# Optimization experiments

Measured on AMD Instinct MI355X. Metric: run time of the kernel, lower is better.

Reference implementation:

```python
import jax, jax.numpy as jnp
import numpy as np

EMBED = 1024
HEADS = 16
HEAD_DIM = EMBED // HEADS


def setup_inputs() -> dict:
    key = jax.random.key(0)
    ks = jax.random.split(key, 8)
    N, S = 4, 2048
    inp = {
        "values": jax.random.normal(ks[0], (N, S, EMBED), dtype=jnp.float32),
        "keys": jax.random.normal(ks[1], (N, S, EMBED), dtype=jnp.float32),
        "queries": jax.random.normal(ks[2], (N, S, EMBED), dtype=jnp.float32),
        # Linear weights stored as [in, out] (torch Linear applies x @ W.T; here W already transposed)
        "W_v": jax.random.normal(ks[3], (EMBED, EMBED), dtype=jnp.float32) / np.sqrt(EMBED),
        "W_k": jax.random.normal(ks[4], (EMBED, EMBED), dtype=jnp.float32) / np.sqrt(EMBED),
        "W_q": jax.random.normal(ks[5], (EMBED, EMBED), dtype=jnp.float32) / np.sqrt(EMBED),
        "W_o": jax.random.normal(ks[6], (EMBED, EMBED), dtype=jnp.float32) / np.sqrt(EMBED),
        "b_o": jax.random.normal(ks[7], (EMBED,), dtype=jnp.float32) * 0.01,
    }
    return inp


def reference(values, keys, queries, W_v, W_k, W_q, W_o, b_o):
    N, q_len, _ = queries.shape
    v = (values @ W_v).reshape(N, -1, HEADS, HEAD_DIM)   # [n, v_len, h, d]
    k = (keys @ W_k).reshape(N, -1, HEADS, HEAD_DIM)     # [n, k_len, h, d]
    q = (queries @ W_q).reshape(N, -1, HEADS, HEAD_DIM)  # [n, q_len, h, d]
    # NOTE: original scales by sqrt(embed_size), not sqrt(head_dim)
    energy = jnp.einsum('nqhd,nkhd->nhqk', q, k) / jnp.sqrt(jnp.float32(EMBED))
    attn = jax.nn.softmax(energy, axis=-1)
    out = jnp.einsum('nhqk,nkhd->nqhd', attn, v).reshape(N, q_len, EMBED)
    return out @ W_o + b_o
```

## Files before the change

kernel.cpp:

```cpp
#include <hip/hip_runtime.h>
#include <hip/hip_bf16.h>
#include <stdint.h>

typedef __attribute__((ext_vector_type(8))) short short8;
typedef __attribute__((ext_vector_type(4))) float f32x4;
typedef unsigned short u16;

#define EMBED 1024
#define SEQ 2048
#define NBATCH 4
#define MROWS (NBATCH * SEQ)

__device__ __forceinline__ u16 f2bf(float f) {
  union { float f; uint32_t u; } v; v.f = f;
  uint32_t r = v.u + 0x7fffu + ((v.u >> 16) & 1u);
  return (u16)(r >> 16);
}

__device__ __forceinline__ uint32_t cvtpk(float lo, float hi) {
  uint32_t r;
  asm("v_cvt_pk_bf16_f32 %0, %1, %2" : "=v"(r) : "v"(lo), "v"(hi));
  return r;
}

__device__ __forceinline__ float vexp2(float x) {
  float r;
  asm("v_exp_f32 %0, %1" : "=v"(r) : "v"(x));
  return r;
}

__device__ __forceinline__ void gld16(const void* g, void* l) {
  __builtin_amdgcn_global_load_lds((const __attribute__((address_space(1))) void*)g,
                                   (__attribute__((address_space(3))) void*)l, 16, 0, 0);
}

__global__ __launch_bounds__(256) void wtrans_kernel(const float* __restrict__ W0,
                                                     const float* __restrict__ W1,
                                                     const float* __restrict__ W2,
                                                     const float* __restrict__ W3,
                                                     u16* __restrict__ T0,
                                                     u16* __restrict__ T1,
                                                     u16* __restrict__ T2,
                                                     u16* __restrict__ T3) {
  int z = blockIdx.z;
  const float* W = z == 0 ? W0 : (z == 1 ? W1 : (z == 2 ? W2 : W3));
  u16* Wt = z == 0 ? T0 : (z == 1 ? T1 : (z == 2 ? T2 : T3));
  __shared__ float tile[32][33];
  int bx = blockIdx.x * 32, by = blockIdx.y * 32;
  int tx = threadIdx.x & 31, ty = threadIdx.x >> 5;
#pragma unroll
  for (int i = 0; i < 32; i += 8)
    tile[ty + i][tx] = W[(size_t)(by + ty + i) * EMBED + bx + tx];
  __syncthreads();
#pragma unroll
  for (int i = 0; i < 32; i += 8)
    Wt[(size_t)(bx + ty + i) * EMBED + by + tx] = f2bf(tile[tx][ty + i]);
}

template <int EPI, bool AF32>
__global__ __launch_bounds__(256) void gemm_bt(const void* __restrict__ Av,
                                               const u16* __restrict__ Bt,
                                               void* __restrict__ outp,
                                               const float* __restrict__ bias,
                                               float oscale) {
  constexpr int K = 1024;
  __shared__ u16 lsA[128 * 64];
  __shared__ u16 lsB[128 * 64];
  const int t = threadIdx.x, l = t & 63, w = t >> 6;
  const int g = l >> 4, r15 = l & 15;
  const int m0 = blockIdx.y * 128, n0 = blockIdx.x * 128;
  const int wm = (w >> 1) * 64, wn = (w & 1) * 64;
  f32x4 acc[4][4] = {};
  const int srow = t >> 3;
  const int sc16 = (t & 7) * 16;

  const u16* Bp[4];
#pragma unroll
  for (int j = 0; j < 4; ++j) {
    int row = srow + j * 32;
    int colswz = (sc16 ^ ((row & 7) << 4)) >> 1;
    Bp[j] = Bt + (size_t)(n0 + row) * K + colswz;
  }

  const u16* Ap[4];
  const float* pA[4];
  float4 ar[4][2];
#pragma unroll
  for (int j = 0; j < 4; ++j) {
    int row = srow + j * 32;
    if (AF32) {
      pA[j] = (const float*)Av + (size_t)(m0 + row) * K + (t & 7) * 8;
    } else {
      int colswz = (sc16 ^ ((row & 7) << 4)) >> 1;
      Ap[j] = (const u16*)Av + (size_t)(m0 + row) * K + colswz;
    }
  }

  auto ALOAD = [&](int k0) {
#pragma unroll
    for (int j = 0; j < 4; ++j) {
      ar[j][0] = *(const float4*)(pA[j] + k0);
      ar[j][1] = *(const float4*)(pA[j] + k0 + 4);
    }
  };
  auto AWRITE = [&]() {
#pragma unroll
    for (int j = 0; j < 4; ++j) {
      int row = srow + j * 32;
      uint4 wv = { cvtpk(ar[j][0].x, ar[j][0].y), cvtpk(ar[j][0].z, ar[j][0].w),
                   cvtpk(ar[j][1].x, ar[j][1].y), cvtpk(ar[j][1].z, ar[j][1].w) };
      *(uint4*)((char*)lsA + row * 128 + (sc16 ^ ((row & 7) << 4))) = wv;
    }
  };

  if (AF32) ALOAD(0);

  for (int k0 = 0; k0 < K; k0 += 64) {
#pragma unroll
    for (int j = 0; j < 4; ++j)
      gld16(Bp[j] + k0, lsB + j * 2048 + w * 512);
    if (AF32) {
      AWRITE();
    } else {
#pragma unroll
      for (int j = 0; j < 4; ++j)
        gld16(Ap[j] + k0, lsA + j * 2048 + w * 512);
    }
    __syncthreads();
    short8 af[2][4], bfv[2][4];
#pragma unroll
    for (int kk = 0; kk < 2; ++kk) {
#pragma unroll
      for (int mi = 0; mi < 4; ++mi) {
        int row = wm + mi * 16 + r15;
        af[kk][mi] = *(const short8*)((const char*)lsA + row * 128 + ((kk * 64 + g * 16) ^ ((row & 7) << 4)));
      }
#pragma unroll
      for (int ni = 0; ni < 4; ++ni) {
        int row = wn + ni * 16 + r15;
        bfv[kk][ni] = *(const short8*)((const char*)lsB + row * 128 + ((kk * 64 + g * 16) ^ ((row & 7) << 4)));
      }
    }
    if (AF32 && k0 + 64 < K) ALOAD(k0 + 64);
#pragma unroll
    for (int kk = 0; kk < 2; ++kk)
#pragma unroll
      for (int mi = 0; mi < 4; ++mi)
#pragma unroll
        for (int ni = 0; ni < 4; ++ni)
          acc[mi][ni] = __builtin_amdgcn_mfma_f32_16x16x32_bf16(af[kk][mi], bfv[kk][ni], acc[mi][ni], 0, 0, 0);
    __syncthreads();
  }

#pragma unroll
  for (int mi = 0; mi < 4; ++mi)
#pragma unroll
    for (int ni = 0; ni < 4; ++ni)
#pragma unroll
      for (int r = 0; r < 4; ++r) {
        int row = m0 + wm + mi * 16 + g * 4 + r;
        int col = n0 + wn + ni * 16 + r15;
        float v = acc[mi][ni][r];
        if (EPI == 0) {
          ((u16*)outp)[(((size_t)(row >> 11) * 16 + (col >> 6)) * SEQ + (row & 2047)) * 64 + (col & 63)] = f2bf(v * oscale);
        } else if (EPI == 1) {
          ((u16*)outp)[(((size_t)(row >> 11) * 16 + (col >> 6)) * 64 + (col & 63)) * SEQ + (row & 2047)] = f2bf(v);
        } else {
          ((float*)outp)[(size_t)row * EMBED + col] = v + bias[col];
        }
      }
}

__global__ __launch_bounds__(256) void attn_kernel(const u16* __restrict__ Q,
                                                   const u16* __restrict__ Kb,
                                                   const u16* __restrict__ Vt,
                                                   u16* __restrict__ AO) {
  __shared__ u16 lsK[2][64 * 64];
  __shared__ u16 lsV[2][64 * 64];
  const int t = threadIdx.x, l = t & 63, w = t >> 6;
  const int g = l >> 4, r15 = l & 15;

  const int flat = blockIdx.x;
  const int work = (flat & 7) * 128 + (flat >> 3);
  const int bh = work >> 4;
  const int q0 = (work & 15) * 128;

  const u16* Qh = Q + (size_t)bh * SEQ * 64;
  const u16* Kh = Kb + (size_t)bh * SEQ * 64;
  const u16* Vh = Vt + (size_t)bh * 64 * SEQ;

  short8 qf[2][2];
#pragma unroll
  for (int qi = 0; qi < 2; ++qi)
#pragma unroll
    for (int dh = 0; dh < 2; ++dh)
      qf[qi][dh] = *(const short8*)&Qh[(size_t)(q0 + w * 32 + qi * 16 + r15) * 64 + dh * 32 + g * 8];

  const short8 kones = { 0x3F80, 0x3F80, 0x3F80, 0x3F80, 0x3F80, 0x3F80, 0x3F80, 0x3F80 };
  f32x4 ssum[2] = {};
  f32x4 oacc[4][2] = {};

  const int srow = t >> 3;
  const int scolb = (t & 7) * 16;

  uint4 vreg[2];

  auto STAGE_K = [&](int buf, int kv0) {
#pragma unroll
    for (int j = 0; j < 2; ++j) {
      int row = j * 32 + srow;
      int colswz = (scolb ^ ((row & 7) << 4)) >> 1;
      gld16(Kh + (size_t)(kv0 + row) * 64 + colswz, &lsK[buf][j * 2048 + w * 512]);
    }
  };
  auto VLOAD = [&](int kv0) {
#pragma unroll
    for (int j = 0; j < 2; ++j) {
      int row = j * 32 + srow;
      vreg[j] = *(const uint4*)(Vh + (size_t)row * SEQ + kv0 + (scolb >> 1));
    }
  };
  auto VSTORE = [&](int buf) {
#pragma unroll
    for (int j = 0; j < 2; ++j) {
      int row = j * 32 + srow;
      int c4 = (row & 7) << 4, c3 = ((row >> 3) & 1) << 3;
      char* base = (char*)&lsV[buf][0] + row * 128 + (scolb ^ c4);
      *(uint2*)(base + c3)       = make_uint2(vreg[j].x, vreg[j].y);
      *(uint2*)(base + (8 ^ c3)) = make_uint2(vreg[j].z, vreg[j].w);
    }
  };

  auto STEP = [&](int buf, bool pre, int a) {
    if (pre) {
      VLOAD((a + 1) * 64);
      STAGE_K(buf ^ 1, (a + 1) * 64);
    }
    const u16* Kc = lsK[buf];
    const u16* Vc = lsV[buf];

    f32x4 sacc[2][4] = {};
    __builtin_amdgcn_s_setprio(1);
#pragma unroll
    for (int c = 0; c < 4; ++c) {
      int krow = c * 16 + r15;
      int sz = (krow & 7) << 4;
#pragma unroll
      for (int dh = 0; dh < 2; ++dh) {
        short8 kf = *(const short8*)((const char*)Kc + krow * 128 + ((dh * 64 + g * 16) ^ sz));
#pragma unroll
        for (int qi = 0; qi < 2; ++qi)
          sacc[qi][c] = __builtin_amdgcn_mfma_f32_16x16x32_bf16(kf, qf[qi][dh], sacc[qi][c], 0, 0, 0);
      }
    }
    __builtin_amdgcn_s_setprio(0);

    short8 pb[2][2];
#pragma unroll
    for (int qi = 0; qi < 2; ++qi) {
#pragma unroll
      for (int c = 0; c < 4; ++c)
#pragma unroll
        for (int r = 0; r < 4; ++r)
          sacc[qi][c][r] = vexp2(sacc[qi][c][r]);
#pragma unroll
      for (int kh = 0; kh < 2; ++kh) {
        union { uint32_t u[4]; short8 s; } pu;
        pu.u[0] = cvtpk(sacc[qi][2 * kh][0],     sacc[qi][2 * kh][1]);
        pu.u[1] = cvtpk(sacc[qi][2 * kh][2],     sacc[qi][2 * kh][3]);
        pu.u[2] = cvtpk(sacc[qi][2 * kh + 1][0], sacc[qi][2 * kh + 1][1]);
        pu.u[3] = cvtpk(sacc[qi][2 * kh + 1][2], sacc[qi][2 * kh + 1][3]);
        pb[qi][kh] = pu.s;
      }
    }

#pragma unroll
    for (int qi = 0; qi < 2; ++qi)
#pragma unroll
      for (int kh = 0; kh < 2; ++kh)
        ssum[qi] = __builtin_amdgcn_mfma_f32_16x16x32_bf16(kones, pb[qi][kh], ssum[qi], 0, 0, 0);

    __builtin_amdgcn_s_setprio(1);
#pragma unroll
    for (int dc = 0; dc < 4; ++dc) {
      int vrow = dc * 16 + r15;
      int sz = ((vrow & 7) << 4) | (((vrow >> 3) & 1) << 3);
      const char* vb = (const char*)Vc + vrow * 128;
#pragma unroll
      for (int kh = 0; kh < 2; ++kh) {
        union { uint2 v[2]; short8 s; } va;
        va.v[0] = *(const uint2*)(vb + ((kh * 64 + 8 * g) ^ sz));
        va.v[1] = *(const uint2*)(vb + ((kh * 64 + 32 + 8 * g) ^ sz));
#pragma unroll
        for (int qi = 0; qi < 2; ++qi)
          oacc[dc][qi] = __builtin_amdgcn_mfma_f32_16x16x32_bf16(va.s, pb[qi][kh], oacc[dc][qi], 0, 0, 0);
      }
    }
    __builtin_amdgcn_s_setprio(0);

    if (pre) VSTORE(buf ^ 1);
    __syncthreads();
  };

  VLOAD(0);
  STAGE_K(0, 0);
  VSTORE(0);
  __syncthreads();

#pragma unroll 1
  for (int pair = 0; pair < 16; ++pair) {
    STEP(0, true, 2 * pair);
    STEP(1, pair != 15, 2 * pair + 1);
  }

  const int nb = bh >> 4, h = bh & 15;
  float inv[2] = { 1.0f / ssum[0][0], 1.0f / ssum[1][0] };
#pragma unroll
  for (int dc = 0; dc < 4; ++dc)
#pragma unroll
    for (int qi = 0; qi < 2; ++qi) {
      int q = q0 + w * 32 + qi * 16 + r15;
      int d = dc * 16 + g * 4;
      uint32_t a = cvtpk(oacc[dc][qi][0] * inv[qi], oacc[dc][qi][1] * inv[qi]);
      uint32_t b = cvtpk(oacc[dc][qi][2] * inv[qi], oacc[dc][qi][3] * inv[qi]);
      uint2* dst = (uint2*)&AO[((size_t)(nb * SEQ + q)) * EMBED + h * 64 + d];
      *dst = make_uint2(a, b);
    }
}

extern "C" void kernel_launch(void* const* d_in, const int* in_sizes, int n_in,
                              void* d_out, int out_size, void* d_ws, size_t ws_size,
                              hipStream_t stream) {
  const float* values  = (const float*)d_in[0];
  const float* keys    = (const float*)d_in[1];
  const float* queries = (const float*)d_in[2];
  const float* W_v = (const float*)d_in[3];
  const float* W_k = (const float*)d_in[4];
  const float* W_q = (const float*)d_in[5];
  const float* W_o = (const float*)d_in[6];
  const float* b_o = (const float*)d_in[7];

  const size_t XSZ = (size_t)MROWS * EMBED;
  const size_t WSZ = (size_t)EMBED * EMBED;
  u16* ws = (u16*)d_ws;
  u16* AO  = ws;
  u16* Wvt = ws + XSZ;
  u16* Wkt = Wvt + WSZ;
  u16* Wqt = Wkt + WSZ;
  u16* Wot = Wqt + WSZ;
  u16* Qb  = Wot + WSZ;
  u16* Kb  = Qb + XSZ;
  u16* Vtb = Kb + XSZ;

  wtrans_kernel<<<dim3(32, 32, 4), 256, 0, stream>>>(W_v, W_k, W_q, W_o, Wvt, Wkt, Wqt, Wot);

  const float QSCALE = 0.03125f * 1.4426950408889634f;
  dim3 gg(EMBED / 128, MROWS / 128);
  gemm_bt<0, true><<<gg, 256, 0, stream>>>(queries, Wqt, Qb, nullptr, QSCALE);
  gemm_bt<0, true><<<gg, 256, 0, stream>>>(keys,    Wkt, Kb, nullptr, 1.0f);
  gemm_bt<1, true><<<gg, 256, 0, stream>>>(values,  Wvt, Vtb, nullptr, 1.0f);

  attn_kernel<<<1024, 256, 0, stream>>>(Qb, Kb, Vtb, AO);

  gemm_bt<2, false><<<gg, 256, 0, stream>>>(AO, Wot, d_out, b_o, 1.0f);
}
```

Before: 254.5 us.

## Pre-convert activations to bf16 and batch QKV projections into one launch

```diff
diff --git a/kernel.cpp b/kernel.cpp
--- a/kernel.cpp
+++ b/kernel.cpp
@@ -4,6 +4,7 @@
 
 typedef __attribute__((ext_vector_type(8))) short short8;
 typedef __attribute__((ext_vector_type(4))) float f32x4;
+typedef __attribute__((ext_vector_type(4))) unsigned short u16x4;
 typedef unsigned short u16;
 
 #define EMBED 1024
@@ -34,35 +35,54 @@
                                    (__attribute__((address_space(3))) void*)l, 16, 0, 0);
 }
 
-__global__ __launch_bounds__(256) void wtrans_kernel(const float* __restrict__ W0,
-                                                     const float* __restrict__ W1,
-                                                     const float* __restrict__ W2,
-                                                     const float* __restrict__ W3,
-                                                     u16* __restrict__ T0,
-                                                     u16* __restrict__ T1,
-                                                     u16* __restrict__ T2,
-                                                     u16* __restrict__ T3) {
-  int z = blockIdx.z;
-  const float* W = z == 0 ? W0 : (z == 1 ? W1 : (z == 2 ? W2 : W3));
-  u16* Wt = z == 0 ? T0 : (z == 1 ? T1 : (z == 2 ? T2 : T3));
-  __shared__ float tile[32][33];
-  int bx = blockIdx.x * 32, by = blockIdx.y * 32;
-  int tx = threadIdx.x & 31, ty = threadIdx.x >> 5;
-#pragma unroll
-  for (int i = 0; i < 32; i += 8)
-    tile[ty + i][tx] = W[(size_t)(by + ty + i) * EMBED + bx + tx];
-  __syncthreads();
-#pragma unroll
-  for (int i = 0; i < 32; i += 8)
-    Wt[(size_t)(bx + ty + i) * EMBED + by + tx] = f2bf(tile[tx][ty + i]);
-}
-
-template <int EPI, bool AF32>
-__global__ __launch_bounds__(256) void gemm_bt(const void* __restrict__ Av,
-                                               const u16* __restrict__ Bt,
-                                               void* __restrict__ outp,
-                                               const float* __restrict__ bias,
-                                               float oscale) {
+__global__ __launch_bounds__(256) void prep_kernel(const float4* __restrict__ a,
+                                                   const float4* __restrict__ b,
+                                                   const float4* __restrict__ c,
+                                                   u16x4* __restrict__ oa,
+                                                   u16x4* __restrict__ ob,
+                                                   u16x4* __restrict__ oc, int n4,
+                                                   const float* __restrict__ W0,
+                                                   const float* __restrict__ W1,
+                                                   const float* __restrict__ W2,
+                                                   const float* __restrict__ W3,
+                                                   u16* __restrict__ T0,
+                                                   u16* __restrict__ T1,
+                                                   u16* __restrict__ T2,
+                                                   u16* __restrict__ T3) {
+  if (blockIdx.x < 1536) {
+    int which = blockIdx.x >> 9;
+    const float4* in = which == 0 ? a : (which == 1 ? b : c);
+    u16x4* out = which == 0 ? oa : (which == 1 ? ob : oc);
+    int stride = 512 * 256;
+    for (int i = (blockIdx.x & 511) * 256 + threadIdx.x; i < n4; i += stride) {
+      float4 v = in[i];
+      u16x4 o = { f2bf(v.x), f2bf(v.y), f2bf(v.z), f2bf(v.w) };
+      out[i] = o;
+    }
+  } else {
+    int id = blockIdx.x - 1536;
+    int z = id >> 10;
+    const float* W = z == 0 ? W0 : (z == 1 ? W1 : (z == 2 ? W2 : W3));
+    u16* Wt = z == 0 ? T0 : (z == 1 ? T1 : (z == 2 ? T2 : T3));
+    __shared__ float tile[32][33];
+    int bx = (id & 31) * 32, by = ((id >> 5) & 31) * 32;
+    int tx = threadIdx.x & 31, ty = threadIdx.x >> 5;
+#pragma unroll
+    for (int i = 0; i < 32; i += 8)
+      tile[ty + i][tx] = W[(size_t)(by + ty + i) * EMBED + bx + tx];
+    __syncthreads();
+#pragma unroll
+    for (int i = 0; i < 32; i += 8)
+      Wt[(size_t)(bx + ty + i) * EMBED + by + tx] = f2bf(tile[tx][ty + i]);
+  }
+}
+
+template <bool DYN>
+__device__ __forceinline__ void gemm_body(const u16* __restrict__ A,
+                                          const u16* __restrict__ Bt,
+                                          void* __restrict__ outp,
+                                          const float* __restrict__ bias,
+                                          float oscale, int epi) {
   constexpr int K = 1024;
   __shared__ u16 lsA[128 * 64];
   __shared__ u16 lsB[128 * 64];
@@ -74,57 +94,20 @@
   const int srow = t >> 3;
   const int sc16 = (t & 7) * 16;
 
-  const u16* Bp[4];
+  const u16* Ap[4]; const u16* Bp[4];
 #pragma unroll
   for (int j = 0; j < 4; ++j) {
     int row = srow + j * 32;
     int colswz = (sc16 ^ ((row & 7) << 4)) >> 1;
+    Ap[j] = A  + (size_t)(m0 + row) * K + colswz;
     Bp[j] = Bt + (size_t)(n0 + row) * K + colswz;
   }
 
-  const u16* Ap[4];
-  const float* pA[4];
-  float4 ar[4][2];
-#pragma unroll
-  for (int j = 0; j < 4; ++j) {
-    int row = srow + j * 32;
-    if (AF32) {
-      pA[j] = (const float*)Av + (size_t)(m0 + row) * K + (t & 7) * 8;
-    } else {
-      int colswz = (sc16 ^ ((row & 7) << 4)) >> 1;
-      Ap[j] = (const u16*)Av + (size_t)(m0 + row) * K + colswz;
-    }
-  }
-
-  auto ALOAD = [&](int k0) {
+  for (int k0 = 0; k0 < K; k0 += 64) {
 #pragma unroll
     for (int j = 0; j < 4; ++j) {
-      ar[j][0] = *(const float4*)(pA[j] + k0);
-      ar[j][1] = *(const float4*)(pA[j] + k0 + 4);
-    }
-  };
-  auto AWRITE = [&]() {
-#pragma unroll
-    for (int j = 0; j < 4; ++j) {
-      int row = srow + j * 32;
-      uint4 wv = { cvtpk(ar[j][0].x, ar[j][0].y), cvtpk(ar[j][0].z, ar[j][0].w),
-                   cvtpk(ar[j][1].x, ar[j][1].y), cvtpk(ar[j][1].z, ar[j][1].w) };
-      *(uint4*)((char*)lsA + row * 128 + (sc16 ^ ((row & 7) << 4))) = wv;
-    }
-  };
-
-  if (AF32) ALOAD(0);
-
-  for (int k0 = 0; k0 < K; k0 += 64) {
-#pragma unroll
-    for (int j = 0; j < 4; ++j)
+      gld16(Ap[j] + k0, lsA + j * 2048 + w * 512);
       gld16(Bp[j] + k0, lsB + j * 2048 + w * 512);
-    if (AF32) {
-      AWRITE();
-    } else {
-#pragma unroll
-      for (int j = 0; j < 4; ++j)
-        gld16(Ap[j] + k0, lsA + j * 2048 + w * 512);
     }
     __syncthreads();
     short8 af[2][4], bfv[2][4];
@@ -141,7 +124,6 @@
         bfv[kk][ni] = *(const short8*)((const char*)lsB + row * 128 + ((kk * 64 + g * 16) ^ ((row & 7) << 4)));
       }
     }
-    if (AF32 && k0 + 64 < K) ALOAD(k0 + 64);
 #pragma unroll
     for (int kk = 0; kk < 2; ++kk)
 #pragma unroll
@@ -161,14 +143,40 @@
         int row = m0 + wm + mi * 16 + g * 4 + r;
         int col = n0 + wn + ni * 16 + r15;
         float v = acc[mi][ni][r];
-        if (EPI == 0) {
-          ((u16*)outp)[(((size_t)(row >> 11) * 16 + (col >> 6)) * SEQ + (row & 2047)) * 64 + (col & 63)] = f2bf(v * oscale);
-        } else if (EPI == 1) {
-          ((u16*)outp)[(((size_t)(row >> 11) * 16 + (col >> 6)) * 64 + (col & 63)) * SEQ + (row & 2047)] = f2bf(v);
+        if (DYN) {
+          if (epi == 0) {
+            ((u16*)outp)[(((size_t)(row >> 11) * 16 + (col >> 6)) * SEQ + (row & 2047)) * 64 + (col & 63)] = f2bf(v * oscale);
+          } else {
+            ((u16*)outp)[(((size_t)(row >> 11) * 16 + (col >> 6)) * 64 + (col & 63)) * SEQ + (row & 2047)] = f2bf(v);
+          }
         } else {
           ((float*)outp)[(size_t)row * EMBED + col] = v + bias[col];
         }
       }
+}
+
+__global__ __launch_bounds__(256) void qkv_gemm(const u16* __restrict__ Xq,
+                                                const u16* __restrict__ Xk,
+                                                const u16* __restrict__ Xv,
+                                                const u16* __restrict__ Wqt,
+                                                const u16* __restrict__ Wkt,
+                                                const u16* __restrict__ Wvt,
+                                                u16* __restrict__ Qb,
+                                                u16* __restrict__ Kb,
+                                                u16* __restrict__ Vtb,
+                                                float qscale) {
+  int z = blockIdx.z;
+  const u16* A  = z == 0 ? Xq : (z == 1 ? Xk : Xv);
+  const u16* Bt = z == 0 ? Wqt : (z == 1 ? Wkt : Wvt);
+  u16* out      = z == 0 ? Qb : (z == 1 ? Kb : Vtb);
+  gemm_body<true>(A, Bt, out, nullptr, z == 0 ? qscale : 1.0f, z == 2 ? 1 : 0);
+}
+
+__global__ __launch_bounds__(256) void gemm_o(const u16* __restrict__ A,
+                                              const u16* __restrict__ Bt,
+                                              float* __restrict__ outp,
+                                              const float* __restrict__ bias) {
+  gemm_body<false>(A, Bt, outp, bias, 1.0f, 2);
 }
 
 __global__ __launch_bounds__(256) void attn_kernel(const u16* __restrict__ Q,
@@ -343,24 +351,30 @@
   const size_t XSZ = (size_t)MROWS * EMBED;
   const size_t WSZ = (size_t)EMBED * EMBED;
   u16* ws = (u16*)d_ws;
-  u16* AO  = ws;
-  u16* Wvt = ws + XSZ;
+  u16* Xv  = ws;
+  u16* Xk  = ws + XSZ;
+  u16* Xq  = ws + 2 * XSZ;
+  u16* Wvt = ws + 3 * XSZ;
   u16* Wkt = Wvt + WSZ;
   u16* Wqt = Wkt + WSZ;
   u16* Wot = Wqt + WSZ;
   u16* Qb  = Wot + WSZ;
   u16* Kb  = Qb + XSZ;
   u16* Vtb = Kb + XSZ;
-
-  wtrans_kernel<<<dim3(32, 32, 4), 256, 0, stream>>>(W_v, W_k, W_q, W_o, Wvt, Wkt, Wqt, Wot);
+  u16* AO  = Xv;
+
+  int n4 = (int)(XSZ / 4);
+  prep_kernel<<<5632, 256, 0, stream>>>((const float4*)values, (const float4*)keys,
+                                        (const float4*)queries,
+                                        (u16x4*)Xv, (u16x4*)Xk, (u16x4*)Xq, n4,
+                                        W_v, W_k, W_q, W_o, Wvt, Wkt, Wqt, Wot);
 
   const float QSCALE = 0.03125f * 1.4426950408889634f;
+  dim3 gq(EMBED / 128, MROWS / 128, 3);
+  qkv_gemm<<<gq, 256, 0, stream>>>(Xq, Xk, Xv, Wqt, Wkt, Wvt, Qb, Kb, Vtb, QSCALE);
+
+  attn_kernel<<<1024, 256, 0, stream>>>(Qb, Kb, Vtb, AO);
+
   dim3 gg(EMBED / 128, MROWS / 128);
-  gemm_bt<0, true><<<gg, 256, 0, stream>>>(queries, Wqt, Qb, nullptr, QSCALE);
-  gemm_bt<0, true><<<gg, 256, 0, stream>>>(keys,    Wkt, Kb, nullptr, 1.0f);
-  gemm_bt<1, true><<<gg, 256, 0, stream>>>(values,  Wvt, Vtb, nullptr, 1.0f);
-
-  attn_kernel<<<1024, 256, 0, stream>>>(Qb, Kb, Vtb, AO);
-
-  gemm_bt<2, false><<<gg, 256, 0, stream>>>(AO, Wot, d_out, b_o, 1.0f);
-}
+  gemm_o<<<gg, 256, 0, stream>>>(AO, Wot, (float*)d_out, b_o);
+}
```

Measured after the change: 230.1 us. -9.6%, faster.
